# Performance work log

Measured on AMD Instinct MI355X. Metric: run time of the kernel, lower is better.

## Reference

```python
import jax, jax.numpy as jnp
import numpy as np

DEPTH = 2
DIM = 512
FF = 2048
INNER = 32
VOCAB = 8192
B = 2
L = 512
LN_EPS = 1e-5


def _layer_norm(x, g, b):
    m = jnp.mean(x, axis=-1, keepdims=True)
    v = jnp.var(x, axis=-1, keepdims=True)
    return (x - m) * jax.lax.rsqrt(v + LN_EPS) * g + b


def _sioconv_layer(x, wa, wx, v_re, v_im, h0_re, h0_im, w_ol):
    # x: [B, L, DIM] float32
    Bb, Ll, _ = x.shape
    I = v_re.shape[0]
    # complex gate a with magnitude sigmoid(log|a|^2)
    af = (x @ wa.T).reshape(Bb, Ll, I, 2)
    a = jax.lax.complex(af[..., 0], af[..., 1])
    m = jnp.square(af[..., 0]) + jnp.square(af[..., 1])
    a = a * jax.lax.rsqrt(m) * jax.nn.sigmoid(jnp.log(m))  # [B,L,I] complex
    # complex input x with magnitude |x| (x * rsqrt(|x|^2) * |x|^2)
    xf = (x @ wx.T).reshape(Bb, Ll, I, 2)
    xc = jax.lax.complex(xf[..., 0], xf[..., 1])
    mx = jnp.square(xf[..., 0]) + jnp.square(xf[..., 1])
    xc = xc * jax.lax.rsqrt(mx) * mx  # [B,L,I] complex
    # cumulative log-decay products: the original's FFT conv of the upper-
    # triangular a_ln against an all-ones matrix is exactly a cumsum along j.
    a_ln = jnp.log(a)  # [B,L,I]
    ii = jnp.arange(Ll)[:, None]
    jj = jnp.arange(Ll)[None, :]
    tri = jnp.where((jj >= ii)[None, None, :, :],
                    jnp.transpose(a_ln, (0, 2, 1))[:, :, None, :],
                    jnp.zeros((), a_ln.dtype))  # [B,I,L,L]: tri[b,d,i,j]=a_ln[b,j,d] for j>=i
    s = jnp.cumsum(tri, axis=3)
    # c[b,d,i,j] = prod_{t=i..j} a[b,t,d] for j>=i; =1 at j=i-1; 0 below.
    c = jnp.where((jj >= ii - 1)[None, None, :, :], jnp.exp(s), jnp.zeros((), s.dtype))
    V = jax.lax.complex(v_re, v_im)
    Vinv = jnp.linalg.inv(V)
    h0 = jax.lax.complex(h0_re, h0_im)  # [I]
    xct = jnp.transpose(xc, (0, 2, 1))  # [B,I,L]
    x_roll = jnp.roll(xct, 1, axis=2).at[:, :, 0].set(h0[None, :])
    # original builds C[b,l,m,n,o] = V diag(c) V^-1 then einsum; contract lazily:
    y = jnp.einsum('ko,bol->bkl', Vinv, x_roll)  # eigenbasis inputs [B,I,L]
    t = jnp.einsum('bkij,bki->bjk', c, y)        # recurrence in eigenbasis [B,L,I]
    h = jnp.einsum('bjk,nk->bjn', t, V)          # back to state basis [B,L,I]
    h = h.at[:, -1, :].add(xc[:, -1, :])         # last step input (others already in c via j=i-1 band)
    return jnp.real(h) @ w_ol.T


def setup_inputs() -> dict:
    key = jax.random.key(0)
    ks = jax.random.split(key, 16)
    f = lambda k, shp: jax.random.normal(k, shp, dtype=jnp.float32)
    return {
        'x': f(ks[0], (B, L, VOCAB)),
        'w_in': f(ks[1], (DIM, VOCAB)) * VOCAB ** -0.5,
        'b_in': jnp.zeros((DIM,), jnp.float32),
        'ln1_g': jnp.ones((DEPTH, DIM), jnp.float32),
        'ln1_b': jnp.zeros((DEPTH, DIM), jnp.float32),
        'wa': f(ks[2], (DEPTH, 2 * INNER, DIM)) * DIM ** -0.5,
        'wx': f(ks[3], (DEPTH, 2 * INNER, DIM)) * DIM ** -0.5,
        'v_re': f(ks[4], (DEPTH, INNER, INNER)),
        'v_im': f(ks[5], (DEPTH, INNER, INNER)),
        'h0_re': f(ks[6], (DEPTH, INNER)),
        'h0_im': f(ks[7], (DEPTH, INNER)),
        'w_ol': f(ks[8], (DEPTH, DIM, INNER)) * INNER ** -0.5,
        'ln2_g': jnp.ones((DEPTH, DIM), jnp.float32),
        'ln2_b': jnp.zeros((DEPTH, DIM), jnp.float32),
        'w1': f(ks[9], (DEPTH, FF, DIM)) * DIM ** -0.5,
        'b1': jnp.zeros((DEPTH, FF), jnp.float32),
        'w2': f(ks[10], (DEPTH, DIM, FF)) * FF ** -0.5,
        'b2': jnp.zeros((DEPTH, DIM), jnp.float32),
        'lnl_g': jnp.ones((DIM,), jnp.float32),
        'lnl_b': jnp.zeros((DIM,), jnp.float32),
        'w_out': f(ks[11], (VOCAB, DIM)) * DIM ** -0.5,
        'b_out': jnp.zeros((VOCAB,), jnp.float32),
    }


def reference(x, w_in, b_in, ln1_g, ln1_b, wa, wx, v_re, v_im, h0_re, h0_im,
              w_ol, ln2_g, ln2_b, w1, b1, w2, b2, lnl_g, lnl_b, w_out, b_out):
    h = x @ w_in.T + b_in  # [B,L,DIM]
    for d in range(DEPTH):
        r = h
        z = _layer_norm(h, ln1_g[d], ln1_b[d])
        z = _sioconv_layer(z, wa[d], wx[d], v_re[d], v_im[d], h0_re[d], h0_im[d], w_ol[d])
        h = z + r
        r = h
        z = _layer_norm(h, ln2_g[d], ln2_b[d])
        z = jax.nn.silu(z @ w1[d].T + b1[d]) @ w2[d].T + b2[d]
        h = z + r
    h = _layer_norm(h, lnl_g, lnl_b)
    return h @ w_out.T + b_out
```

## Files before the change

### kernel.cpp

```cpp
#include <hip/hip_runtime.h>
#include <stdint.h>

#define DEPTHC 2
#define DIMC   512
#define FFC    2048
#define INNERC 32
#define VOCABC 8192
#define BC     2
#define LC     512
#define NTOK   1024

typedef _Float16 f16;
typedef __attribute__((ext_vector_type(8))) _Float16 f16x8;
typedef __attribute__((ext_vector_type(4))) float f32x4;

__device__ __forceinline__ float2 cmul2(float2 a, float2 b){
    return make_float2(a.x*b.x - a.y*b.y, a.x*b.y + a.y*b.x);
}
__device__ __forceinline__ float2 cadd2(float2 a, float2 b){
    return make_float2(a.x + b.x, a.y + b.y);
}

__device__ __forceinline__ void gl_lds16(const void* g, void* l){
    __builtin_amdgcn_global_load_lds(
        (const __attribute__((address_space(1))) unsigned int*)g,
        (__attribute__((address_space(3))) unsigned int*)l, 16, 0, 0);
}

__global__ __launch_bounds__(256) void k_prep(
    const float* __restrict__ s0, const float* __restrict__ s1,
    const float* __restrict__ s2, const float* __restrict__ s3,
    const float* __restrict__ s4,
    f16* __restrict__ d0, f16* __restrict__ d1, f16* __restrict__ d2,
    f16* __restrict__ d3, f16* __restrict__ d4,
    int n0, int n1, int n2, int n3, int n4,
    const float* __restrict__ v_re, const float* __restrict__ v_im,
    const float* __restrict__ h0re, const float* __restrict__ h0im,
    float2* __restrict__ vinv, float2* __restrict__ h0c)
{
    __shared__ float2 M[32][64];
    if (blockIdx.x < 2){
        const int d = blockIdx.x;
        const int tid = threadIdx.x;
        const int c = tid & 63;
        const int wv = tid >> 6;
        if (tid < 32) h0c[d*32 + tid] = make_float2(h0re[d*32 + tid], h0im[d*32 + tid]);
#pragma unroll
        for (int rr = 0; rr < 8; ++rr){
            int r = wv*8 + rr;
            float re, im;
            if (c < 32){ re = v_re[d*1024 + r*32 + c]; im = v_im[d*1024 + r*32 + c]; }
            else       { re = (c - 32 == r) ? 1.f : 0.f; im = 0.f; }
            M[r][c] = make_float2(re, im);
        }
        __syncthreads();
#pragma unroll 1
        for (int col = 0; col < 32; ++col){
            float2 prow = M[col][c];
            float pvx = __shfl(prow.x, col, 64);
            float pvy = __shfl(prow.y, col, 64);
            float dm = pvx*pvx + pvy*pvy;
            float ir = pvx/dm, ii = -pvy/dm;
            float2 nv = make_float2(prow.x*ir - prow.y*ii, prow.x*ii + prow.y*ir);
#pragma unroll
            for (int rr = 0; rr < 8; ++rr){
                int r = wv*8 + rr;
                if (r == col) continue;
                float2 f  = M[r][col];
                float2 m0 = M[r][c];
                m0.x -= f.x*nv.x - f.y*nv.y;
                m0.y -= f.x*nv.y + f.y*nv.x;
                M[r][c] = m0;
            }
            __syncthreads();
        }
        if (c >= 32){
#pragma unroll
            for (int rr = 0; rr < 8; ++rr){
                int r = wv*8 + rr;
                float2 dv = M[r][r];
                float dm = dv.x*dv.x + dv.y*dv.y;
                float ir = dv.x/dm, ii = -dv.y/dm;
                float2 m0 = M[r][c];
                vinv[d*1024 + r*32 + (c - 32)] =
                    make_float2(m0.x*ir - m0.y*ii, m0.x*ii + m0.y*ir);
            }
        }
        return;
    }
    long long i = ((long long)(blockIdx.x - 2) * 256 + threadIdx.x) * 4;
    const float* s; f16* d;
    if (i < n0){ s = s0; d = d0; }
    else { i -= n0;
        if (i < n1){ s = s1; d = d1; }
        else { i -= n1;
            if (i < n2){ s = s2; d = d2; }
            else { i -= n2;
                if (i < n3){ s = s3; d = d3; }
                else { i -= n3; if (i >= n4) return; s = s4; d = d4; }
            }
        }
    }
    float4 v = *(const float4*)(s + i);
    union { f16 h[4]; float2 f2; } u;
    u.h[0] = (f16)v.x; u.h[1] = (f16)v.y; u.h[2] = (f16)v.z; u.h[3] = (f16)v.w;
    *(float2*)(d + i) = u.f2;
}

template<int MT, int NT, int MODE>
__global__ __launch_bounds__(256) void k_gemmT(
    const f16* __restrict__ A, const f16* __restrict__ Bw,
    void* __restrict__ C, const float* __restrict__ bias,
    int N, int K, int klen, int partStride)
{
    constexpr int RM = MT/32, RN = NT/32;
    __shared__ __align__(16) f16 As[MT*64];
    __shared__ __align__(16) f16 Bs[NT*64];
    const int tid = threadIdx.x;
    const int m0 = blockIdx.y * MT;
    const int n0 = blockIdx.x * NT;
    const int kbeg = blockIdx.z * klen;
    const int l = tid & 63;
    const int w = tid >> 6;
    const int fr = l & 15;
    const int fq = l >> 4;
    const int wm = (w >> 1) * (MT/2);
    const int wn = (w & 1) * (NT/2);
    const f16* gA = A  + (size_t)(m0 + (tid >> 3)) * K + kbeg + (tid & 7) * 8;
    const f16* gB = Bw + (size_t)(n0 + (tid >> 3)) * K + kbeg + (tid & 7) * 8;
    const size_t rowskip = (size_t)32 * K;
    f16* lA = As + tid * 8;
    f16* lB = Bs + tid * 8;
    f32x4 acc[RM][RN];
#pragma unroll
    for (int i = 0; i < RM; ++i)
#pragma unroll
        for (int j = 0; j < RN; ++j)
            acc[i][j] = (f32x4){0.f, 0.f, 0.f, 0.f};
    for (int kk = 0; kk < klen; kk += 64){
        __syncthreads();
#pragma unroll
        for (int i = 0; i < MT/32; ++i) gl_lds16(gA + i*rowskip, lA + i*2048);
#pragma unroll
        for (int i = 0; i < NT/32; ++i) gl_lds16(gB + i*rowskip, lB + i*2048);
        gA += 64; gB += 64;
        __syncthreads();
#pragma unroll
        for (int h = 0; h < 2; ++h){
            f16x8 af[RM], bf[RN];
#pragma unroll
            for (int i = 0; i < RM; ++i) af[i] = *(const f16x8*)(As + (wm + 16*i + fr) * 64 + h*32 + fq * 8);
#pragma unroll
            for (int j = 0; j < RN; ++j) bf[j] = *(const f16x8*)(Bs + (wn + 16*j + fr) * 64 + h*32 + fq * 8);
#pragma unroll
            for (int i = 0; i < RM; ++i)
#pragma unroll
                for (int j = 0; j < RN; ++j)
                    acc[i][j] = __builtin_amdgcn_mfma_f32_16x16x32_f16(af[i], bf[j], acc[i][j], 0, 0, 0);
        }
    }
#pragma unroll
    for (int i = 0; i < RM; ++i)
#pragma unroll
        for (int j = 0; j < RN; ++j)
#pragma unroll
            for (int r = 0; r < 4; ++r){
                int row = m0 + wm + 16*i + fq*4 + r;
                int col = n0 + wn + 16*j + fr;
                if (MODE == 1){
                    ((f16*)C + (size_t)blockIdx.z * partStride)[(size_t)row * N + col] = (f16)acc[i][j][r];
                } else if (MODE == 0){
                    ((float*)C)[(size_t)row * N + col] = acc[i][j][r] + bias[col];
                } else {
                    float v = acc[i][j][r] + bias[col];
                    ((f16*)C)[(size_t)row * N + col] = (f16)(v / (1.f + __expf(-v)));
                }
            }
}

__global__ __launch_bounds__(256) void k_reduce8(
    float* __restrict__ out, const f16* __restrict__ part,
    const float* __restrict__ bias, const float* __restrict__ res, int n)
{
    int i = (blockIdx.x * 256 + threadIdx.x) * 2;
    if (i >= n) return;
    float v0 = bias[i & (DIMC - 1)], v1 = bias[(i + 1) & (DIMC - 1)];
    if (res){ v0 += res[i]; v1 += res[i + 1]; }
#pragma unroll
    for (int z = 0; z < 8; ++z){
        union { uint32_t u; f16 h[2]; } q;
        q.u = *(const uint32_t*)(part + (size_t)z * n + i);
        v0 += (float)q.h[0]; v1 += (float)q.h[1];
    }
    *(float2*)(out + i) = make_float2(v0, v1);
}

__global__ __launch_bounds__(128) void k_red8_ln(
    const f16* __restrict__ part, const float* __restrict__ bias,
    const float* __restrict__ res, const float* __restrict__ g,
    const float* __restrict__ b, f16* __restrict__ out, int n)
{
    int row = blockIdx.x;
    int tid = threadIdx.x;
    __shared__ float sw[2], qw[2];
    float v[4]; float s = 0.f, q = 0.f;
#pragma unroll
    for (int j = 0; j < 4; ++j){
        int c = tid + 128*j;
        int idx = row*DIMC + c;
        float t = bias[c] + res[idx];
#pragma unroll
        for (int z = 0; z < 8; ++z) t += (float)part[(size_t)z * n + idx];
        v[j] = t; s += t; q += t*t;
    }
    for (int off = 32; off; off >>= 1){ s += __shfl_down(s, off, 64); q += __shfl_down(q, off, 64); }
    if ((tid & 63) == 0){ sw[tid >> 6] = s; qw[tid >> 6] = q; }
    __syncthreads();
    float S = sw[0] + sw[1], Q = qw[0] + qw[1];
    float m = S / DIMC;
    float rstd = rsqrtf(Q / DIMC - m*m + 1e-5f);
#pragma unroll
    for (int j = 0; j < 4; ++j){
        int c = tid + 128*j;
        out[(size_t)row*DIMC + c] = (f16)((v[j] - m)*rstd*g[c] + b[c]);
    }
}

__global__ __launch_bounds__(128) void k_siogate(
    const float* __restrict__ H, const float* __restrict__ g, const float* __restrict__ b,
    const float* __restrict__ wa, const float* __restrict__ wx,
    float2* __restrict__ a_t, float2* __restrict__ xc)
{
    __shared__ float zs[4][DIMC];
    __shared__ float sc[4][128];
    __shared__ float rs2[2], rq2[2];
    int tid = threadIdx.x;
    int r0 = blockIdx.x * 4;
    for (int gg = 0; gg < 4; ++gg){
        const float* xr = H + (size_t)(r0 + gg) * DIMC;
        float v[4]; float s = 0.f, q = 0.f;
#pragma unroll
        for (int j = 0; j < 4; ++j){ v[j] = xr[tid + 128*j]; s += v[j]; q += v[j]*v[j]; }
        for (int off = 32; off; off >>= 1){ s += __shfl_down(s, off, 64); q += __shfl_down(q, off, 64); }
        if ((tid & 63) == 0){ rs2[tid >> 6] = s; rq2[tid >> 6] = q; }
        __syncthreads();
        float m = (rs2[0] + rs2[1]) / DIMC;
        float var = (rq2[0] + rq2[1]) / DIMC - m*m;
        float rst = rsqrtf(var + 1e-5f);
#pragma unroll
        for (int j = 0; j < 4; ++j){ int c = tid + 128*j; zs[gg][c] = (v[j] - m)*rst*g[c] + b[c]; }
        __syncthreads();
    }
    const float* wrow = (tid < 64) ? (wa + (size_t)tid * DIMC) : (wx + (size_t)(tid - 64) * DIMC);
    float dot[4] = {0.f, 0.f, 0.f, 0.f};
    for (int c = 0; c < DIMC; c += 4){
        float4 wv = *(const float4*)(wrow + c);
#pragma unroll
        for (int gg = 0; gg < 4; ++gg){
            float4 zv = *(const float4*)(&zs[gg][c]);
            dot[gg] += wv.x*zv.x + wv.y*zv.y + wv.z*zv.z + wv.w*zv.w;
        }
    }
#pragma unroll
    for (int gg = 0; gg < 4; ++gg) sc[gg][tid] = dot[gg];
    __syncthreads();
    int gg = tid >> 5, k = tid & 31;
    int row = r0 + gg;
    int bb = row >> 9, t = row & 511;
    float re = sc[gg][2*k], im = sc[gg][2*k + 1];
    float m2 = re*re + im*im;
    float sa = rsqrtf(m2) * (m2 / (1.f + m2));
    a_t[(size_t)(bb*INNERC + k)*LC + t] = make_float2(re*sa, im*sa);
    float xr2 = sc[gg][64 + 2*k], xi2 = sc[gg][64 + 2*k + 1];
    float mx = xr2*xr2 + xi2*xi2;
    float sx = sqrtf(mx);
    xc[(size_t)row*INNERC + k] = make_float2(xr2*sx, xi2*sx);
}

__global__ __launch_bounds__(64) void k_scan(
    const float2* __restrict__ a_t, const float2* __restrict__ xc,
    const float2* __restrict__ vinv, const float2* __restrict__ h0c,
    float2* __restrict__ e)
{
    int bk = blockIdx.x;
    int l = threadIdx.x;
    int bb = bk >> 5, k = bk & 31;
    float2 vrow[32];
#pragma unroll
    for (int o = 0; o < 32; ++o) vrow[o] = vinv[k*32 + o];
    int base = bk * LC + l * 8;
    float2 av[8], wv[8];
#pragma unroll
    for (int j = 0; j < 8; ++j) av[j] = a_t[base + j];
#pragma unroll
    for (int j = 0; j < 8; ++j){
        int t = l*8 + j;
        const float2* src = (t == 0) ? h0c : (xc + (size_t)(bb*LC + t - 1) * INNERC);
        float2 acc = make_float2(0.f, 0.f);
#pragma unroll
        for (int o = 0; o < 32; o += 2){
            float4 qq = *(const float4*)(src + o);
            acc.x += vrow[o].x*qq.x - vrow[o].y*qq.y;
            acc.y += vrow[o].x*qq.y + vrow[o].y*qq.x;
            acc.x += vrow[o+1].x*qq.z - vrow[o+1].y*qq.w;
            acc.y += vrow[o+1].x*qq.w + vrow[o+1].y*qq.z;
        }
        wv[j] = acc;
    }
    float2 A = make_float2(1.f, 0.f), Bc = make_float2(0.f, 0.f);
#pragma unroll
    for (int j = 0; j < 8; ++j){
        Bc = cmul2(av[j], cadd2(Bc, wv[j]));
        A  = cmul2(av[j], A);
    }
    for (int off = 1; off < 64; off <<= 1){
        float Apx = __shfl_up(A.x,  off, 64), Apy = __shfl_up(A.y,  off, 64);
        float Bpx = __shfl_up(Bc.x, off, 64), Bpy = __shfl_up(Bc.y, off, 64);
        if (l >= off){
            float2 Ap = make_float2(Apx, Apy), Bp = make_float2(Bpx, Bpy);
            Bc = cadd2(cmul2(A, Bp), Bc);
            A  = cmul2(A, Ap);
        }
    }
    float ex = __shfl_up(Bc.x, 1, 64), ey = __shfl_up(Bc.y, 1, 64);
    float2 ecur = (l == 0) ? make_float2(0.f, 0.f) : make_float2(ex, ey);
    size_t obase = ((size_t)bb*LC + l*8) * INNERC + k;
#pragma unroll
    for (int j = 0; j < 8; ++j){
        ecur = cmul2(av[j], cadd2(ecur, wv[j]));
        e[obase + (size_t)j * INNERC] = ecur;
    }
}

__global__ __launch_bounds__(128) void k_siout_ln(
    const float2* __restrict__ e, const float2* __restrict__ xc,
    const float* __restrict__ vre, const float* __restrict__ vim,
    const float* __restrict__ wol, const float* __restrict__ res,
    const float* __restrict__ g2, const float* __restrict__ b2,
    float* __restrict__ hout, f16* __restrict__ zout)
{
    int bt = blockIdx.x;
    int tid = threadIdx.x;
    __shared__ float hr[INNERC];
    __shared__ float2 er[INNERC];
    __shared__ float sw[2], qw[2];
    if (tid < 32) er[tid] = e[(size_t)bt*INNERC + tid];
    __syncthreads();
    if (tid < 32){
        const float* vrr = vre + tid*INNERC;
        const float* vir = vim + tid*INNERC;
        float acc = xc[(size_t)bt*INNERC + tid].x;
#pragma unroll
        for (int k2 = 0; k2 < 32; ++k2) acc += vrr[k2]*er[k2].x - vir[k2]*er[k2].y;
        hr[tid] = acc;
    }
    __syncthreads();
    float v[4]; float s = 0.f, q = 0.f;
#pragma unroll
    for (int j = 0; j < 4; ++j){
        int n = tid + 128*j;
        float val = res[(size_t)bt*DIMC + n];
        const float* wr = wol + (size_t)n * INNERC;
#pragma unroll
        for (int i = 0; i < 32; ++i) val += hr[i]*wr[i];
        hout[(size_t)bt*DIMC + n] = val;
        v[j] = val; s += val; q += val*val;
    }
    for (int off = 32; off; off >>= 1){ s += __shfl_down(s, off, 64); q += __shfl_down(q, off, 64); }
    if ((tid & 63) == 0){ sw[tid >> 6] = s; qw[tid >> 6] = q; }
    __syncthreads();
    float S = sw[0] + sw[1], Q = qw[0] + qw[1];
    float m = S / DIMC;
    float rstd = rsqrtf(Q / DIMC - m*m + 1e-5f);
#pragma unroll
    for (int j = 0; j < 4; ++j){
        int n = tid + 128*j;
        zout[(size_t)bt*DIMC + n] = (f16)((v[j] - m)*rstd*g2[n] + b2[n]);
    }
}

extern "C" void kernel_launch(void* const* d_in, const int* in_sizes, int n_in,
                              void* d_out, int out_size, void* d_ws, size_t ws_size,
                              hipStream_t stream)
{
    const float* x     = (const float*)d_in[0];
    const float* w_in  = (const float*)d_in[1];
    const float* b_in  = (const float*)d_in[2];
    const float* ln1_g = (const float*)d_in[3];
    const float* ln1_b = (const float*)d_in[4];
    const float* wa    = (const float*)d_in[5];
    const float* wx    = (const float*)d_in[6];
    const float* v_re  = (const float*)d_in[7];
    const float* v_im  = (const float*)d_in[8];
    const float* h0_re = (const float*)d_in[9];
    const float* h0_im = (const float*)d_in[10];
    const float* w_ol  = (const float*)d_in[11];
    const float* ln2_g = (const float*)d_in[12];
    const float* ln2_b = (const float*)d_in[13];
    const float* w1    = (const float*)d_in[14];
    const float* b1    = (const float*)d_in[15];
    const float* w2    = (const float*)d_in[16];
    const float* b2    = (const float*)d_in[17];
    const float* lnl_g = (const float*)d_in[18];
    const float* lnl_b = (const float*)d_in[19];
    const float* w_out = (const float*)d_in[20];
    const float* b_out = (const float*)d_in[21];

    char* p = (char*)d_ws;
    f16* xb   = (f16*)p;   p += (size_t)NTOK * VOCABC * 2;
    f16* wib  = (f16*)p;   p += (size_t)DIMC * VOCABC * 2;
    f16* wob  = (f16*)p;   p += (size_t)VOCABC * DIMC * 2;
    f16* w1b  = (f16*)p;   p += (size_t)DEPTHC * FFC * DIMC * 2;
    f16* w2b  = (f16*)p;   p += (size_t)DEPTHC * DIMC * FFC * 2;
    float* h1 = (float*)p; p += (size_t)NTOK * DIMC * 4;
    float* h2 = (float*)p; p += (size_t)NTOK * DIMC * 4;
    float* h3 = (float*)p; p += (size_t)NTOK * DIMC * 4;
    f16* zb   = (f16*)p;   p += (size_t)NTOK * DIMC * 2;
    f16* ffb  = (f16*)p;   p += (size_t)NTOK * FFC * 2;
    f16* pbuf = (f16*)p;   p += (size_t)8 * NTOK * DIMC * 2;
    float2* a_t = (float2*)p; p += (size_t)BC * INNERC * LC * 8;
    float2* xc  = (float2*)p; p += (size_t)NTOK * INNERC * 8;
    float2* ev  = (float2*)p; p += (size_t)NTOK * INNERC * 8;
    float2* vinv = (float2*)p; p += (size_t)DEPTHC * INNERC * INNERC * 8;
    float2* h0c  = (float2*)p; p += (size_t)DEPTHC * INNERC * 8;

    {
        const int n0 = NTOK*VOCABC, n1 = DIMC*VOCABC, n2 = DEPTHC*FFC*DIMC,
                  n3 = DEPTHC*DIMC*FFC, n4 = VOCABC*DIMC;
        int blocks = (n0 + n1 + n2 + n3 + n4) / 1024 + 2;
        k_prep<<<blocks, 256, 0, stream>>>(x, w_in, w1, w2, w_out,
                                           xb, wib, w1b, w2b, wob, n0, n1, n2, n3, n4,
                                           v_re, v_im, h0_re, h0_im, vinv, h0c);
    }

    {
        dim3 g(DIMC/128, NTOK/64, 8);
        k_gemmT<64,128,1><<<g, 256, 0, stream>>>(xb, wib, pbuf, nullptr, DIMC, VOCABC, VOCABC/8, NTOK*DIMC);
    }

    for (int d = 0; d < DEPTHC; ++d){
        float* cur = (d == 0) ? h1 : h3;
        float* hb  = h2;
        const float* redBias = (d == 0) ? b_in : (b2 + (d-1)*DIMC);
        const float* redRes  = (d == 0) ? nullptr : h2;
        k_reduce8<<<(NTOK*DIMC)/512, 256, 0, stream>>>(cur, pbuf, redBias, redRes, NTOK*DIMC);
        k_siogate<<<NTOK/4, 128, 0, stream>>>(cur, ln1_g + d*DIMC, ln1_b + d*DIMC,
                                              wa + (size_t)d*2*INNERC*DIMC,
                                              wx + (size_t)d*2*INNERC*DIMC, a_t, xc);
        k_scan<<<BC*INNERC, 64, 0, stream>>>(a_t, xc, vinv + d*INNERC*INNERC, h0c + d*INNERC, ev);
        k_siout_ln<<<NTOK, 128, 0, stream>>>(ev, xc, v_re + d*INNERC*INNERC, v_im + d*INNERC*INNERC,
                                             w_ol + (size_t)d*DIMC*INNERC, cur,
                                             ln2_g + d*DIMC, ln2_b + d*DIMC, hb, zb);
        {
            dim3 g(FFC/128, NTOK/64, 1);
            k_gemmT<64,128,2><<<g, 256, 0, stream>>>(zb, w1b + (size_t)d*FFC*DIMC, ffb, b1 + d*FFC,
                                                     FFC, DIMC, DIMC, 0);
        }
        {
            dim3 g(DIMC/128, NTOK/64, 8);
            k_gemmT<64,128,1><<<g, 256, 0, stream>>>(ffb, w2b + (size_t)d*DIMC*FFC, pbuf, nullptr,
                                                     DIMC, FFC, FFC/8, NTOK*DIMC);
        }
    }
    k_red8_ln<<<NTOK, 128, 0, stream>>>(pbuf, b2 + (DEPTHC-1)*DIMC, h2, lnl_g, lnl_b, zb, NTOK*DIMC);
    {
        dim3 g(VOCABC/128, NTOK/128, 1);
        k_gemmT<128,128,0><<<g, 256, 0, stream>>>(zb, wob, (float*)d_out, b_out, VOCABC, DIMC, DIMC, 0);
    }
    (void)in_sizes; (void)n_in; (void)out_size; (void)ws_size;
}
```

Baseline: 364.8 us.

## Fuse split-K reduction into siogate and enlarge GEMM tiles with fewer K splits

Folds the split-K partial-sum reduction, bias and residual into the siogate LayerNorm kernel, so one launch goes away and the reduced hidden state is not re-read from memory. The gate kernel now handles two rows per 256-thread block instead of four rows per 128-thread block. The GEMMs move from 64x128 to 128x128 tiles, and the FF2 GEMM drops from 8 to 4 K-splits, which shrinks partial-buffer traffic. The cost is fewer blocks in the grid, which may lower occupancy and parallelism on the small GEMMs.

```diff
diff --git a/kernel.cpp b/kernel.cpp
--- a/kernel.cpp
+++ b/kernel.cpp
@@ -178,27 +178,83 @@
             }
 }
 
-__global__ __launch_bounds__(256) void k_reduce8(
-    float* __restrict__ out, const f16* __restrict__ part,
-    const float* __restrict__ bias, const float* __restrict__ res, int n)
-{
-    int i = (blockIdx.x * 256 + threadIdx.x) * 2;
-    if (i >= n) return;
-    float v0 = bias[i & (DIMC - 1)], v1 = bias[(i + 1) & (DIMC - 1)];
-    if (res){ v0 += res[i]; v1 += res[i + 1]; }
-#pragma unroll
-    for (int z = 0; z < 8; ++z){
-        union { uint32_t u; f16 h[2]; } q;
-        q.u = *(const uint32_t*)(part + (size_t)z * n + i);
-        v0 += (float)q.h[0]; v1 += (float)q.h[1];
-    }
-    *(float2*)(out + i) = make_float2(v0, v1);
-}
-
-__global__ __launch_bounds__(128) void k_red8_ln(
+__global__ __launch_bounds__(256) void k_siogate(
+    const f16* __restrict__ part, const float* __restrict__ bias,
+    const float* __restrict__ res, float* __restrict__ hout,
+    const float* __restrict__ g, const float* __restrict__ b,
+    const float* __restrict__ wa, const float* __restrict__ wx,
+    float2* __restrict__ a_t, float2* __restrict__ xc, int nz)
+{
+    __shared__ float zs[2][DIMC];
+    __shared__ float sc[2][128];
+    __shared__ float rs[2][4], rq[2][4];
+    const int tid = threadIdx.x;
+    const int r0 = blockIdx.x * 2;
+    const int c = tid * 2;
+    float v0g[2], v1g[2];
+#pragma unroll
+    for (int gg = 0; gg < 2; ++gg){
+        int row = r0 + gg;
+        size_t idx = (size_t)row*DIMC + c;
+        float v0 = bias[c], v1 = bias[c+1];
+        if (res){ v0 += res[idx]; v1 += res[idx+1]; }
+        for (int z = 0; z < nz; ++z){
+            union { uint32_t u; f16 h[2]; } q;
+            q.u = *(const uint32_t*)(part + (size_t)z*(NTOK*DIMC) + idx);
+            v0 += (float)q.h[0]; v1 += (float)q.h[1];
+        }
+        hout[idx] = v0; hout[idx+1] = v1;
+        v0g[gg] = v0; v1g[gg] = v1;
+        float s = v0 + v1, qq = v0*v0 + v1*v1;
+        for (int off = 32; off; off >>= 1){ s += __shfl_down(s, off, 64); qq += __shfl_down(qq, off, 64); }
+        if ((tid & 63) == 0){ rs[gg][tid >> 6] = s; rq[gg][tid >> 6] = qq; }
+    }
+    __syncthreads();
+#pragma unroll
+    for (int gg = 0; gg < 2; ++gg){
+        float S = rs[gg][0]+rs[gg][1]+rs[gg][2]+rs[gg][3];
+        float Q = rq[gg][0]+rq[gg][1]+rq[gg][2]+rq[gg][3];
+        float m = S / DIMC;
+        float rst = rsqrtf(Q / DIMC - m*m + 1e-5f);
+        zs[gg][c]   = (v0g[gg] - m)*rst*g[c]   + b[c];
+        zs[gg][c+1] = (v1g[gg] - m)*rst*g[c+1] + b[c+1];
+    }
+    __syncthreads();
+    {
+        const int rr = tid >> 7;
+        const int o  = tid & 127;
+        const float* wrow = (o < 64) ? (wa + (size_t)o * DIMC) : (wx + (size_t)(o - 64) * DIMC);
+        float dot = 0.f;
+        for (int cc = 0; cc < DIMC; cc += 4){
+            float4 wv = *(const float4*)(wrow + cc);
+            float4 zv = *(const float4*)(&zs[rr][cc]);
+            dot += wv.x*zv.x + wv.y*zv.y + wv.z*zv.z + wv.w*zv.w;
+        }
+        sc[rr][o] = dot;
+    }
+    __syncthreads();
+    if (tid < 128){
+        int rr = tid >> 6, which = (tid >> 5) & 1, k = tid & 31;
+        int row = r0 + rr;
+        int bb = row >> 9, t = row & 511;
+        if (which == 0){
+            float re = sc[rr][2*k], im = sc[rr][2*k + 1];
+            float m2 = re*re + im*im;
+            float sa = rsqrtf(m2) * (m2 / (1.f + m2));
+            a_t[(size_t)(bb*INNERC + k)*LC + t] = make_float2(re*sa, im*sa);
+        } else {
+            float xr2 = sc[rr][64 + 2*k], xi2 = sc[rr][64 + 2*k + 1];
+            float mx = xr2*xr2 + xi2*xi2;
+            float sx = sqrtf(mx);
+            xc[(size_t)row*INNERC + k] = make_float2(xr2*sx, xi2*sx);
+        }
+    }
+}
+
+__global__ __launch_bounds__(128) void k_red_ln(
     const f16* __restrict__ part, const float* __restrict__ bias,
     const float* __restrict__ res, const float* __restrict__ g,
-    const float* __restrict__ b, f16* __restrict__ out, int n)
+    const float* __restrict__ b, f16* __restrict__ out, int n, int nz)
 {
     int row = blockIdx.x;
     int tid = threadIdx.x;
@@ -209,8 +265,7 @@
         int c = tid + 128*j;
         int idx = row*DIMC + c;
         float t = bias[c] + res[idx];
-#pragma unroll
-        for (int z = 0; z < 8; ++z) t += (float)part[(size_t)z * n + idx];
+        for (int z = 0; z < nz; ++z) t += (float)part[(size_t)z * n + idx];
         v[j] = t; s += t; q += t*t;
     }
     for (int off = 32; off; off >>= 1){ s += __shfl_down(s, off, 64); q += __shfl_down(q, off, 64); }
@@ -224,57 +279,6 @@
         int c = tid + 128*j;
         out[(size_t)row*DIMC + c] = (f16)((v[j] - m)*rstd*g[c] + b[c]);
     }
-}
-
-__global__ __launch_bounds__(128) void k_siogate(
-    const float* __restrict__ H, const float* __restrict__ g, const float* __restrict__ b,
-    const float* __restrict__ wa, const float* __restrict__ wx,
-    float2* __restrict__ a_t, float2* __restrict__ xc)
-{
-    __shared__ float zs[4][DIMC];
-    __shared__ float sc[4][128];
-    __shared__ float rs2[2], rq2[2];
-    int tid = threadIdx.x;
-    int r0 = blockIdx.x * 4;
-    for (int gg = 0; gg < 4; ++gg){
-        const float* xr = H + (size_t)(r0 + gg) * DIMC;
-        float v[4]; float s = 0.f, q = 0.f;
-#pragma unroll
-        for (int j = 0; j < 4; ++j){ v[j] = xr[tid + 128*j]; s += v[j]; q += v[j]*v[j]; }
-        for (int off = 32; off; off >>= 1){ s += __shfl_down(s, off, 64); q += __shfl_down(q, off, 64); }
-        if ((tid & 63) == 0){ rs2[tid >> 6] = s; rq2[tid >> 6] = q; }
-        __syncthreads();
-        float m = (rs2[0] + rs2[1]) / DIMC;
-        float var = (rq2[0] + rq2[1]) / DIMC - m*m;
-        float rst = rsqrtf(var + 1e-5f);
-#pragma unroll
-        for (int j = 0; j < 4; ++j){ int c = tid + 128*j; zs[gg][c] = (v[j] - m)*rst*g[c] + b[c]; }
-        __syncthreads();
-    }
-    const float* wrow = (tid < 64) ? (wa + (size_t)tid * DIMC) : (wx + (size_t)(tid - 64) * DIMC);
-    float dot[4] = {0.f, 0.f, 0.f, 0.f};
-    for (int c = 0; c < DIMC; c += 4){
-        float4 wv = *(const float4*)(wrow + c);
-#pragma unroll
-        for (int gg = 0; gg < 4; ++gg){
-            float4 zv = *(const float4*)(&zs[gg][c]);
-            dot[gg] += wv.x*zv.x + wv.y*zv.y + wv.z*zv.z + wv.w*zv.w;
-        }
-    }
-#pragma unroll
-    for (int gg = 0; gg < 4; ++gg) sc[gg][tid] = dot[gg];
-    __syncthreads();
-    int gg = tid >> 5, k = tid & 31;
-    int row = r0 + gg;
-    int bb = row >> 9, t = row & 511;
-    float re = sc[gg][2*k], im = sc[gg][2*k + 1];
-    float m2 = re*re + im*im;
-    float sa = rsqrtf(m2) * (m2 / (1.f + m2));
-    a_t[(size_t)(bb*INNERC + k)*LC + t] = make_float2(re*sa, im*sa);
-    float xr2 = sc[gg][64 + 2*k], xi2 = sc[gg][64 + 2*k + 1];
-    float mx = xr2*xr2 + xi2*xi2;
-    float sx = sqrtf(mx);
-    xc[(size_t)row*INNERC + k] = make_float2(xr2*sx, xi2*sx);
 }
 
 __global__ __launch_bounds__(64) void k_scan(
@@ -434,8 +438,8 @@
     }
 
     {
-        dim3 g(DIMC/128, NTOK/64, 8);
-        k_gemmT<64,128,1><<<g, 256, 0, stream>>>(xb, wib, pbuf, nullptr, DIMC, VOCABC, VOCABC/8, NTOK*DIMC);
+        dim3 g(DIMC/128, NTOK/128, 8);
+        k_gemmT<128,128,1><<<g, 256, 0, stream>>>(xb, wib, pbuf, nullptr, DIMC, VOCABC, VOCABC/8, NTOK*DIMC);
     }
 
     for (int d = 0; d < DEPTHC; ++d){
@@ -443,26 +447,27 @@
         float* hb  = h2;
         const float* redBias = (d == 0) ? b_in : (b2 + (d-1)*DIMC);
         const float* redRes  = (d == 0) ? nullptr : h2;
-        k_reduce8<<<(NTOK*DIMC)/512, 256, 0, stream>>>(cur, pbuf, redBias, redRes, NTOK*DIMC);
-        k_siogate<<<NTOK/4, 128, 0, stream>>>(cur, ln1_g + d*DIMC, ln1_b + d*DIMC,
+        const int nz = (d == 0) ? 8 : 4;
+        k_siogate<<<NTOK/2, 256, 0, stream>>>(pbuf, redBias, redRes, cur,
+                                              ln1_g + d*DIMC, ln1_b + d*DIMC,
                                               wa + (size_t)d*2*INNERC*DIMC,
-                                              wx + (size_t)d*2*INNERC*DIMC, a_t, xc);
+                                              wx + (size_t)d*2*INNERC*DIMC, a_t, xc, nz);
         k_scan<<<BC*INNERC, 64, 0, stream>>>(a_t, xc, vinv + d*INNERC*INNERC, h0c + d*INNERC, ev);
         k_siout_ln<<<NTOK, 128, 0, stream>>>(ev, xc, v_re + d*INNERC*INNERC, v_im + d*INNERC*INNERC,
                                              w_ol + (size_t)d*DIMC*INNERC, cur,
                                              ln2_g + d*DIMC, ln2_b + d*DIMC, hb, zb);
         {
-            dim3 g(FFC/128, NTOK/64, 1);
-            k_gemmT<64,128,2><<<g, 256, 0, stream>>>(zb, w1b + (size_t)d*FFC*DIMC, ffb, b1 + d*FFC,
-                                                     FFC, DIMC, DIMC, 0);
+            dim3 g(FFC/128, NTOK/128, 1);
+            k_gemmT<128,128,2><<<g, 256, 0, stream>>>(zb, w1b + (size_t)d*FFC*DIMC, ffb, b1 + d*FFC,
+                                                      FFC, DIMC, DIMC, 0);
         }
         {
-            dim3 g(DIMC/128, NTOK/64, 8);
-            k_gemmT<64,128,1><<<g, 256, 0, stream>>>(ffb, w2b + (size_t)d*DIMC*FFC, pbuf, nullptr,
-                                                     DIMC, FFC, FFC/8, NTOK*DIMC);
-        }
-    }
-    k_red8_ln<<<NTOK, 128, 0, stream>>>(pbuf, b2 + (DEPTHC-1)*DIMC, h2, lnl_g, lnl_b, zb, NTOK*DIMC);
+            dim3 g(DIMC/128, NTOK/128, 4);
+            k_gemmT<128,128,1><<<g, 256, 0, stream>>>(ffb, w2b + (size_t)d*DIMC*FFC, pbuf, nullptr,
+                                                      DIMC, FFC, FFC/4, NTOK*DIMC);
+        }
+    }
+    k_red_ln<<<NTOK, 128, 0, stream>>>(pbuf, b2 + (DEPTHC-1)*DIMC, h2, lnl_g, lnl_b, zb, NTOK*DIMC, 4);
     {
         dim3 g(VOCABC/128, NTOK/128, 1);
         k_gemmT<128,128,0><<<g, 256, 0, stream>>>(zb, wob, (float*)d_out, b_out, VOCABC, DIMC, DIMC, 0);
```

New measurement: 401.5 us. +10.1%, slower.
